# Kernel tuning notes

Hardware: AMD Instinct MI355X
Metric: run time of the kernel (lower is better)

The kernel has to match this reference:

```python
import jax, jax.numpy as jnp
import numpy as np

NUM_BITS = 8
SEQ, BATCH, INPUT, HIDDEN = 512, 256, 256, 256


def fake_quant(w):
    # symmetric per-tensor uniform fake-quantization with straight-through estimator
    qmax = 2.0 ** (NUM_BITS - 1) - 1.0
    scale = jnp.max(jnp.abs(w)) / qmax
    wq = jnp.round(w / scale) * scale
    return w + jax.lax.stop_gradient(wq - w)


def gru_cell(x, h, w_ih, w_hh, b_ih, b_hh):
    # x: [B, I], h: [B, H]; w_ih: [3H, I], w_hh: [3H, H]
    gi = x @ fake_quant(w_ih).T + b_ih  # [B, 3H]
    gh = h @ fake_quant(w_hh).T + b_hh  # [B, 3H]
    i_r, i_z, i_n = jnp.split(gi, 3, axis=-1)
    h_r, h_z, h_n = jnp.split(gh, 3, axis=-1)
    r = jax.nn.sigmoid(i_r + h_r)
    z = jax.nn.sigmoid(i_z + h_z)
    n = jnp.tanh(i_n + r * h_n)
    return (1.0 - z) * n + z * h


def setup_inputs() -> dict:
    key = jax.random.key(0)
    ks = jax.random.split(key, 9)
    s1 = 1.0 / np.sqrt(HIDDEN)
    inp = {
        "x": jax.random.normal(ks[0], (SEQ, BATCH, INPUT), dtype=jnp.float32),
        "h1": jnp.zeros((BATCH, HIDDEN), dtype=jnp.float32),
        "h2": jnp.zeros((BATCH, HIDDEN), dtype=jnp.float32),
        "w_ih1": jax.random.uniform(ks[1], (3 * HIDDEN, INPUT), jnp.float32, -s1, s1),
        "w_hh1": jax.random.uniform(ks[2], (3 * HIDDEN, HIDDEN), jnp.float32, -s1, s1),
        "b_ih1": jax.random.uniform(ks[3], (3 * HIDDEN,), jnp.float32, -s1, s1),
        "b_hh1": jax.random.uniform(ks[4], (3 * HIDDEN,), jnp.float32, -s1, s1),
        "w_ih2": jax.random.uniform(ks[5], (3 * HIDDEN, HIDDEN), jnp.float32, -s1, s1),
        "w_hh2": jax.random.uniform(ks[6], (3 * HIDDEN, HIDDEN), jnp.float32, -s1, s1),
        "b_ih2": jax.random.uniform(ks[7], (3 * HIDDEN,), jnp.float32, -s1, s1),
        "b_hh2": jax.random.uniform(ks[8], (3 * HIDDEN,), jnp.float32, -s1, s1),
    }
    return inp


def reference(x, h1, h2, w_ih1, w_hh1, b_ih1, b_hh1, w_ih2, w_hh2, b_ih2, b_hh2):
    def step(carry, x_t):
        h1, h2 = carry
        h1 = gru_cell(x_t, h1, w_ih1, w_hh1, b_ih1, b_hh1)
        h2 = gru_cell(h1, h2, w_ih2, w_hh2, b_ih2, b_hh2)
        return (h1, h2), None

    (h1, h2), _ = jax.lax.scan(step, (h1, h2), x)
    return h2
```

## Files before the change

### kernel.cpp

```cpp
#include <hip/hip_runtime.h>
#include <hip/hip_fp16.h>
#include <cstdint>

typedef _Float16 half8 __attribute__((ext_vector_type(8)));
typedef _Float16 half4 __attribute__((ext_vector_type(4)));
typedef float f32x4 __attribute__((ext_vector_type(4)));

#define MFMA_F16 __builtin_amdgcn_mfma_f32_16x16x32_f16
#define PIN(x)   asm volatile("" : "+v"(x))
#define LD_RLX(p)   __hip_atomic_load((p),  __ATOMIC_RELAXED, __HIP_MEMORY_SCOPE_AGENT)
#define LD_ACQ(p)   __hip_atomic_load((p),  __ATOMIC_ACQUIRE, __HIP_MEMORY_SCOPE_AGENT)
#define ST_REL(p,v) __hip_atomic_store((p),(v), __ATOMIC_RELEASE, __HIP_MEMORY_SCOPE_AGENT)

__device__ __forceinline__ float fast_rcp(float x){
#if __has_builtin(__builtin_amdgcn_rcpf)
  return __builtin_amdgcn_rcpf(x);
#else
  return 1.0f/x;
#endif
}
__device__ __forceinline__ float fast_exp2(float x){
#if __has_builtin(__builtin_amdgcn_exp2f)
  return __builtin_amdgcn_exp2f(x);
#else
  return exp2f(x);
#endif
}
__device__ __forceinline__ float sigm_f(float x){
  return fast_rcp(1.0f + fast_exp2(-1.44269504f*x));
}
__device__ __forceinline__ float tanh_fast(float x){
  float e = fast_exp2(-2.88539008f*x);
  return fmaf(2.0f, fast_rcp(1.0f + e), -1.0f);
}

__device__ __forceinline__ void bar_weak(){
  asm volatile("s_waitcnt lgkmcnt(0)" ::: "memory");
  __builtin_amdgcn_s_barrier();
  asm volatile("" ::: "memory");
}
__device__ __forceinline__ void bar_strong(){
  asm volatile("s_waitcnt vmcnt(0) lgkmcnt(0)" ::: "memory");
  __builtin_amdgcn_s_barrier();
  asm volatile("" ::: "memory");
}

__device__ __forceinline__ half8 qfrag(const float* __restrict__ W, int tile,
                                       int kb, int l, float scale){
  int row = tile*16 + (l & 15);
  int k0  = kb*32 + (l >> 4)*8;
  const float4* p = (const float4*)&W[row*256 + k0];
  float4 a = p[0], b = p[1];
  half8 h;
  h[0] = (_Float16)(rintf(a.x/scale)*scale);
  h[1] = (_Float16)(rintf(a.y/scale)*scale);
  h[2] = (_Float16)(rintf(a.z/scale)*scale);
  h[3] = (_Float16)(rintf(a.w/scale)*scale);
  h[4] = (_Float16)(rintf(b.x/scale)*scale);
  h[5] = (_Float16)(rintf(b.y/scale)*scale);
  h[6] = (_Float16)(rintf(b.z/scale)*scale);
  h[7] = (_Float16)(rintf(b.w/scale)*scale);
  return h;
}

__global__ __launch_bounds__(256) void k_maxabs(
    const float* __restrict__ w0, const float* __restrict__ w1,
    const float* __restrict__ w2, const float* __restrict__ w3,
    int n, int* __restrict__ slots)
{
  const float* srcs[4] = {w0, w1, w2, w3};
  int m    = blockIdx.x >> 5;
  int part = blockIdx.x & 31;
  const float* w = srcs[m];
  float loc = 0.0f;
  for (int i = part*256 + threadIdx.x; i < n; i += 32*256)
    loc = fmaxf(loc, fabsf(w[i]));
  for (int off = 32; off; off >>= 1)
    loc = fmaxf(loc, __shfl_down(loc, off, 64));
  __shared__ float red[4];
  int wv = threadIdx.x >> 6;
  if ((threadIdx.x & 63) == 0) red[wv] = loc;
  __syncthreads();
  if (threadIdx.x == 0) {
    float mx = fmaxf(fmaxf(red[0], red[1]), fmaxf(red[2], red[3]));
    atomicMax(&slots[m], __float_as_int(mx));
  }
}

__global__ __launch_bounds__(256) void k_xcast(
    const float* __restrict__ x, _Float16* __restrict__ xh)
{
  int n = blockIdx.x*256 + threadIdx.x;
  int t   = n >> 13;
  int rem = n & 8191;
  int bg  = rem >> 5;
  int k8  = rem & 31;
  const float4* src = (const float4*)&x[((size_t)t*256 + bg)*256 + k8*8];
  float4 v0 = src[0], v1 = src[1];
  half8 hv;
  hv[0] = (_Float16)v0.x; hv[1] = (_Float16)v0.y;
  hv[2] = (_Float16)v0.z; hv[3] = (_Float16)v0.w;
  hv[4] = (_Float16)v1.x; hv[5] = (_Float16)v1.y;
  hv[6] = (_Float16)v1.z; hv[7] = (_Float16)v1.w;
  int bb = bg >> 4, b = bg & 15, kb = k8 >> 2, lane = (k8 & 3)*16 + b;
  *(half8*)&xh[(size_t)t*65536 + (size_t)bb*4096 + kb*512 + lane*8] = hv;
}

__global__ __launch_bounds__(512, 2) void k_pipe(
    const _Float16* __restrict__ xh,
    const float* __restrict__ wih1, const float* __restrict__ bih1,
    _Float16* __restrict__ gi1, const float* __restrict__ whh1,
    const float* __restrict__ bhh1, float* __restrict__ hc1,
    _Float16* __restrict__ h1seq,
    const float* __restrict__ wih2, const float* __restrict__ bih2,
    const float* __restrict__ bhh2, const float* __restrict__ whh2,
    float* __restrict__ hc2, _Float16* __restrict__ gi2,
    const int* __restrict__ slots,
    int* __restrict__ flag0, int* __restrict__ flag1,
    int* __restrict__ flag2, int* __restrict__ flag3)
{
  __shared__ __align__(16) _Float16 hl[2][4096];
  __shared__ __align__(16) _Float16 wn_l[16384];
  const int role = blockIdx.x;
  const int tid  = threadIdx.x;
  const int w = tid >> 6, l = tid & 63, q = l >> 4, c16 = l & 15;

  if (role >= 32) {
    const bool G1 = (role >= 64);
    const int id = G1 ? role - 64 : role - 32;
    const int bb = id >> 1, par = id & 1;
    const float*    Wsrc = G1 ? wih1  : wih2;
    const float*    bihp = G1 ? bih1  : bih2;
    const float*    bhhp = G1 ? bhh1  : bhh2;
    const _Float16* Asrc = G1 ? xh    : h1seq;
    _Float16*       gout = G1 ? gi1   : gi2;
    const float sc = __int_as_float(slots[G1 ? 0 : 2]) * (1.0f/127.0f);

    float bR[2], bZ[2], bN[2];
    half8 wr[2][8], wz[2][8], wn[2][8];
    #pragma unroll
    for (int nt = 0; nt < 2; nt++) {
      const int j = w*32 + nt*16 + c16;
      bR[nt] = bihp[j]       + bhhp[j];
      bZ[nt] = bihp[256 + j] + bhhp[256 + j];
      bN[nt] = bihp[512 + j];
      #pragma unroll
      for (int kb = 0; kb < 8; kb++) {
        wr[nt][kb] = qfrag(Wsrc,      2*w + nt, kb, l, sc);  PIN(wr[nt][kb]);
        wz[nt][kb] = qfrag(Wsrc, 16 + 2*w + nt, kb, l, sc);  PIN(wz[nt][kb]);
        wn[nt][kb] = qfrag(Wsrc, 32 + 2*w + nt, kb, l, sc);  PIN(wn[nt][kb]);
      }
    }

    for (int g = par; g < 32; g += 2) {
      const int t0 = g*16;
      if (tid == 0) {
        if (!G1) {
          while (LD_RLX(&flag1[bb]) < t0 + 16) __builtin_amdgcn_s_sleep(10);
          if (g >= 4)
            while (LD_RLX(&flag3[bb]) < (g - 3)*16) __builtin_amdgcn_s_sleep(10);
          (void)LD_ACQ(&flag1[bb]);
        } else if (g >= 4) {
          while (LD_RLX(&flag1[bb]) < (g - 3)*16) __builtin_amdgcn_s_sleep(10);
          (void)LD_ACQ(&flag1[bb]);
        }
      }
      __syncthreads();
      for (int t = t0; t < t0 + 16; t++) {
        const _Float16* ap = Asrc + (size_t)t*65536 + (size_t)bb*4096 + l*8;
        f32x4 aR[2], aZ[2], aN[2];
        #pragma unroll
        for (int nt = 0; nt < 2; nt++) {
          aR[nt] = (f32x4){0.f,0.f,0.f,0.f};
          aZ[nt] = (f32x4){0.f,0.f,0.f,0.f};
          aN[nt] = (f32x4){0.f,0.f,0.f,0.f};
        }
        #pragma unroll
        for (int kb = 0; kb < 8; kb++) {
          half8 a = *(const half8*)&ap[kb*512];
          #pragma unroll
          for (int nt = 0; nt < 2; nt++) {
            aR[nt] = MFMA_F16(a, wr[nt][kb], aR[nt], 0, 0, 0);
            aZ[nt] = MFMA_F16(a, wz[nt][kb], aZ[nt], 0, 0, 0);
            aN[nt] = MFMA_F16(a, wn[nt][kb], aN[nt], 0, 0, 0);
          }
        }
        const size_t trow = (size_t)(t & 63);
        #pragma unroll
        for (int nt = 0; nt < 2; nt++) {
          _Float16* op = gout + (trow*256 + (2*w + nt)*16 + bb)*768 + l*12;
          half4 vR, vZ, vN;
          #pragma unroll
          for (int i = 0; i < 4; i++) {
            vR[i] = (_Float16)(aR[nt][i] + bR[nt]);
            vZ[i] = (_Float16)(aZ[nt][i] + bZ[nt]);
            vN[i] = (_Float16)(aN[nt][i] + bN[nt]);
          }
          *(half4*)(op)     = vR;
          *(half4*)(op + 4) = vZ;
          *(half4*)(op + 8) = vN;
        }
      }
      __syncthreads();
      if (tid == 0) {
        if (G1) ST_REL(&flag0[bb*2 + par], t0 + 16);
        else    ST_REL(&flag2[bb*2 + par], t0 + 16);
      }
    }
    return;
  }

  const bool L1 = (role < 16);
  const int bb = L1 ? role : role - 16;
  const int b0 = bb * 16;
  const _Float16* gi = L1 ? gi1 : gi2;
  const float* Wf    = L1 ? whh1 : whh2;
  const float* bhh   = L1 ? bhh1 : bhh2;
  float* hcarry      = L1 ? hc1 : hc2;
  const float sc     = __int_as_float(slots[L1 ? 1 : 3]) * (1.0f/127.0f);

  {
    int n = tid*8;
    int b = n >> 8, k = n & 255;
    const float4* s4 = (const float4*)&hcarry[(size_t)(b0 + b)*256 + k];
    float4 v0 = s4[0], v1 = s4[1];
    half8 hv;
    hv[0] = (_Float16)v0.x; hv[1] = (_Float16)v0.y;
    hv[2] = (_Float16)v0.z; hv[3] = (_Float16)v0.w;
    hv[4] = (_Float16)v1.x; hv[5] = (_Float16)v1.y;
    hv[6] = (_Float16)v1.z; hv[7] = (_Float16)v1.w;
    *(half8*)&hl[0][(k >> 5)*512 + (((k >> 3) & 3)*16 + b)*8] = hv;
  }

  float bN[2];
  float hprev[2][4];
  half8 wr[2][8], wz[2][8], wn[2][6];
  int   wr_off[2];
  int   gil[2];
  #pragma unroll
  for (int nt = 0; nt < 2; nt++) {
    const int j = w*32 + nt*16 + c16;
    bN[nt] = bhh[512 + j];
    #pragma unroll
    for (int i = 0; i < 4; i++)
      hprev[nt][i] = hcarry[(size_t)(b0 + q*4 + i)*256 + j];
    #pragma unroll
    for (int kb = 0; kb < 8; kb++) {
      wr[nt][kb] = qfrag(Wf,      2*w + nt, kb, l, sc);  PIN(wr[nt][kb]);
      wz[nt][kb] = qfrag(Wf, 16 + 2*w + nt, kb, l, sc);  PIN(wz[nt][kb]);
    }
    #pragma unroll
    for (int kb = 2; kb < 8; kb++) {
      wn[nt][kb-2] = qfrag(Wf, 32 + 2*w + nt, kb, l, sc);  PIN(wn[nt][kb-2]);
    }
    #pragma unroll
    for (int kb = 0; kb < 2; kb++)
      *(half8*)&wn_l[((w*2 + nt)*2 + kb)*512 + l*8] =
          qfrag(Wf, 32 + 2*w + nt, kb, l, sc);
    wr_off[nt] = (j >> 5)*512 + ((j >> 3) & 3)*128 + (j & 7);
    gil[nt]    = ((2*w + nt)*16 + bb)*768 + l*12;
  }
  _Float16* hq = L1 ? (h1seq + (size_t)bb*4096 + tid*8) : (_Float16*)nullptr;

  __syncthreads();
  half4 pR[2], pZ[2], pN[2];
  int cur = 0;
  for (int t = 0; t < 512; t++) {
    if ((t & 15) == 0) {
      if (tid == 0) {
        int* f = L1 ? &flag0[bb*2 + ((t >> 4) & 1)]
                    : &flag2[bb*2 + ((t >> 4) & 1)];
        while (LD_RLX(f) < t + 16) __builtin_amdgcn_s_sleep(10);
        (void)LD_ACQ(f);
      }
      __syncthreads();
      const int tm = t & 63;
      const _Float16* gbase = gi + (size_t)tm*196608;
      #pragma unroll
      for (int nt = 0; nt < 2; nt++) {
        const _Float16* gp = gbase + gil[nt];
        pR[nt] = *(const half4*)(gp);
        pZ[nt] = *(const half4*)(gp + 4);
        pN[nt] = *(const half4*)(gp + 8);
      }
    }
    half4 vR[2], vZ[2], vN[2];
    #pragma unroll
    for (int nt = 0; nt < 2; nt++) {
      vR[nt] = pR[nt]; vZ[nt] = pZ[nt]; vN[nt] = pN[nt];
    }

    f32x4 aR[2], aZ[2], aN[2];
    #pragma unroll
    for (int nt = 0; nt < 2; nt++) {
      aR[nt] = (f32x4){0.f,0.f,0.f,0.f};
      aZ[nt] = (f32x4){0.f,0.f,0.f,0.f};
      aN[nt] = (f32x4){0.f,0.f,0.f,0.f};
    }
    #pragma unroll
    for (int kb = 0; kb < 8; kb++) {
      half8 a = *(const half8*)&hl[cur][kb*512 + l*8];
      #pragma unroll
      for (int nt = 0; nt < 2; nt++) {
        half8 bn = (kb < 2)
            ? *(const half8*)&wn_l[((w*2 + nt)*2 + kb)*512 + l*8]
            : wn[nt][kb-2];
        aR[nt] = MFMA_F16(a, wr[nt][kb], aR[nt], 0, 0, 0);
        aZ[nt] = MFMA_F16(a, wz[nt][kb], aZ[nt], 0, 0, 0);
        aN[nt] = MFMA_F16(a, bn,         aN[nt], 0, 0, 0);
      }
    }

    if (((t + 1) & 15) != 0) {
      const int tn = (t + 1) & 63;
      const _Float16* gbase = gi + (size_t)tn*196608;
      #pragma unroll
      for (int nt = 0; nt < 2; nt++) {
        const _Float16* gp = gbase + gil[nt];
        pR[nt] = *(const half4*)(gp);
        pZ[nt] = *(const half4*)(gp + 4);
        pN[nt] = *(const half4*)(gp + 8);
      }
    }

    const int nxt = cur ^ 1;
    #pragma unroll
    for (int nt = 0; nt < 2; nt++) {
      #pragma unroll
      for (int i = 0; i < 4; i++) {
        float r  = sigm_f(aR[nt][i] + (float)vR[nt][i]);
        float z  = sigm_f(aZ[nt][i] + (float)vZ[nt][i]);
        float nn = tanh_fast((float)vN[nt][i] + r*(aN[nt][i] + bN[nt]));
        float hp = nn + z*(hprev[nt][i] - nn);
        hprev[nt][i] = hp;
        hl[nxt][wr_off[nt] + (q*4 + i)*8] = (_Float16)hp;
      }
    }

    if ((t & 15) == 0 && t > 0) {
      bar_strong();
      if (tid == 0) {
        if (L1) ST_REL(&flag1[bb], t);
        else    ST_REL(&flag3[bb], t);
      }
    } else {
      bar_weak();
    }
    if (L1)
      *(half8*)&hq[(size_t)t*65536] = *(const half8*)&hl[nxt][tid*8];
    cur = nxt;
  }
  bar_strong();
  if (tid == 0) {
    if (L1) ST_REL(&flag1[bb], 512);
    else    ST_REL(&flag3[bb], 512);
  }

  #pragma unroll
  for (int nt = 0; nt < 2; nt++) {
    const int j = w*32 + nt*16 + c16;
    #pragma unroll
    for (int i = 0; i < 4; i++)
      hcarry[(size_t)(b0 + q*4 + i)*256 + j] = hprev[nt][i];
  }
}

extern "C" void kernel_launch(void* const* d_in, const int* in_sizes, int n_in,
                              void* d_out, int out_size, void* d_ws, size_t ws_size,
                              hipStream_t stream)
{
  const float* x     = (const float*)d_in[0];
  const float* h1_0  = (const float*)d_in[1];
  const float* h2_0  = (const float*)d_in[2];
  const float* w_ih1 = (const float*)d_in[3];
  const float* w_hh1 = (const float*)d_in[4];
  const float* b_ih1 = (const float*)d_in[5];
  const float* b_hh1 = (const float*)d_in[6];
  const float* w_ih2 = (const float*)d_in[7];
  const float* w_hh2 = (const float*)d_in[8];
  const float* b_ih2 = (const float*)d_in[9];
  const float* b_hh2 = (const float*)d_in[10];

  char* ws = (char*)d_ws;
  size_t off = 0;
  auto alloc = [&](size_t bytes) -> void* {
    void* p = ws + off; off += (bytes + 255) & ~(size_t)255; return p;
  };
  int*      slots   = (int*)     alloc(16);
  float*    hc1     = (float*)   alloc(256*256*4);
  float*    hc2     = (float*)   alloc(256*256*4);
  int*      flag0   = (int*)     alloc(32*4);
  int*      flag1   = (int*)     alloc(16*4);
  int*      flag2   = (int*)     alloc(32*4);
  int*      flag3   = (int*)     alloc(16*4);
  _Float16* gi1     = (_Float16*)alloc((size_t)64*393216);
  _Float16* h1seq   = (_Float16*)alloc((size_t)512*131072);
  _Float16* gi2     = (_Float16*)alloc((size_t)64*393216);
  _Float16* xhbuf   = (_Float16*)alloc((size_t)512*131072);

  k_maxabs<<<128, 256, 0, stream>>>(w_ih1, w_hh1, w_ih2, w_hh2, 196608, slots);
  k_xcast <<<16384, 256, 0, stream>>>(x, xhbuf);
  (void)hipMemcpyAsync(hc1, h1_0, 256*256*4, hipMemcpyDeviceToDevice, stream);
  (void)hipMemcpyAsync(hc2, h2_0, 256*256*4, hipMemcpyDeviceToDevice, stream);

  k_pipe<<<96, 512, 0, stream>>>(xhbuf, w_ih1, b_ih1, gi1, w_hh1, b_hh1,
                                 hc1, h1seq, w_ih2, b_ih2, b_hh2, w_hh2,
                                 hc2, gi2, slots, flag0, flag1, flag2, flag3);

  (void)hipMemcpyAsync(d_out, hc2, 256*256*4, hipMemcpyDeviceToDevice, stream);
}
```

Measured before the change: 1.338 ms.

## Process two batch groups per recurrent block with interleaved MFMA and gate phases

Each recurrent block now handles two 16-row batch groups instead of one, halving the recurrent block count (grid goes from 96 to 80). The MFMA phase of one group is interleaved with the gate/activation phase of the other so that matrix and transcendental work can overlap across the serial time loop. All of W_n now lives in registers, so the LDS copy of part of it is dropped. In exchange each block does twice the per-step work on fewer CUs, uses more registers, and waits on two producer flags.

```diff
diff --git a/kernel.cpp b/kernel.cpp
--- a/kernel.cpp
+++ b/kernel.cpp
@@ -119,15 +119,14 @@
     int* __restrict__ flag0, int* __restrict__ flag1,
     int* __restrict__ flag2, int* __restrict__ flag3)
 {
-  __shared__ __align__(16) _Float16 hl[2][4096];
-  __shared__ __align__(16) _Float16 wn_l[16384];
+  __shared__ __align__(16) _Float16 hl[8192];
   const int role = blockIdx.x;
   const int tid  = threadIdx.x;
   const int w = tid >> 6, l = tid & 63, q = l >> 4, c16 = l & 15;
 
-  if (role >= 32) {
-    const bool G1 = (role >= 64);
-    const int id = G1 ? role - 64 : role - 32;
+  if (role >= 16) {
+    const bool G1 = (role >= 48);
+    const int id = G1 ? role - 48 : role - 16;
     const int bb = id >> 1, par = id & 1;
     const float*    Wsrc = G1 ? wih1  : wih2;
     const float*    bihp = G1 ? bih1  : bih2;
@@ -210,87 +209,66 @@
     return;
   }
 
-  const bool L1 = (role < 16);
-  const int bb = L1 ? role : role - 16;
-  const int b0 = bb * 16;
+  const bool L1 = (role < 8);
+  const int pb = L1 ? role*2 : (role - 8)*2;
   const _Float16* gi = L1 ? gi1 : gi2;
   const float* Wf    = L1 ? whh1 : whh2;
   const float* bhh   = L1 ? bhh1 : bhh2;
   float* hcarry      = L1 ? hc1 : hc2;
   const float sc     = __int_as_float(slots[L1 ? 1 : 3]) * (1.0f/127.0f);
+  int* fAcq = L1 ? flag0 : flag2;
+  int* fPub = L1 ? flag1 : flag3;
+  _Float16* hl0 = hl;
+  _Float16* hl1 = hl + 4096;
 
   {
     int n = tid*8;
     int b = n >> 8, k = n & 255;
-    const float4* s4 = (const float4*)&hcarry[(size_t)(b0 + b)*256 + k];
-    float4 v0 = s4[0], v1 = s4[1];
-    half8 hv;
-    hv[0] = (_Float16)v0.x; hv[1] = (_Float16)v0.y;
-    hv[2] = (_Float16)v0.z; hv[3] = (_Float16)v0.w;
-    hv[4] = (_Float16)v1.x; hv[5] = (_Float16)v1.y;
-    hv[6] = (_Float16)v1.z; hv[7] = (_Float16)v1.w;
-    *(half8*)&hl[0][(k >> 5)*512 + (((k >> 3) & 3)*16 + b)*8] = hv;
+    int dst = (k >> 5)*512 + (((k >> 3) & 3)*16 + b)*8;
+    #pragma unroll
+    for (int bbi = 0; bbi < 2; bbi++) {
+      const float4* s4 = (const float4*)&hcarry[(size_t)((pb+bbi)*16 + b)*256 + k];
+      float4 v0 = s4[0], v1 = s4[1];
+      half8 hv;
+      hv[0] = (_Float16)v0.x; hv[1] = (_Float16)v0.y;
+      hv[2] = (_Float16)v0.z; hv[3] = (_Float16)v0.w;
+      hv[4] = (_Float16)v1.x; hv[5] = (_Float16)v1.y;
+      hv[6] = (_Float16)v1.z; hv[7] = (_Float16)v1.w;
+      *(half8*)&hl[bbi*4096 + dst] = hv;
+    }
   }
 
   float bN[2];
-  float hprev[2][4];
-  half8 wr[2][8], wz[2][8], wn[2][6];
+  float hprev[2][2][4];
+  half8 wr[2][8], wz[2][8], wn[2][8];
   int   wr_off[2];
-  int   gil[2];
+  int   gil[2][2];
   #pragma unroll
   for (int nt = 0; nt < 2; nt++) {
     const int j = w*32 + nt*16 + c16;
     bN[nt] = bhh[512 + j];
     #pragma unroll
-    for (int i = 0; i < 4; i++)
-      hprev[nt][i] = hcarry[(size_t)(b0 + q*4 + i)*256 + j];
+    for (int bbi = 0; bbi < 2; bbi++) {
+      #pragma unroll
+      for (int i = 0; i < 4; i++)
+        hprev[bbi][nt][i] = hcarry[(size_t)((pb+bbi)*16 + q*4 + i)*256 + j];
+      gil[bbi][nt] = ((2*w + nt)*16 + (pb+bbi))*768 + l*12;
+    }
     #pragma unroll
     for (int kb = 0; kb < 8; kb++) {
       wr[nt][kb] = qfrag(Wf,      2*w + nt, kb, l, sc);  PIN(wr[nt][kb]);
       wz[nt][kb] = qfrag(Wf, 16 + 2*w + nt, kb, l, sc);  PIN(wz[nt][kb]);
-    }
-    #pragma unroll
-    for (int kb = 2; kb < 8; kb++) {
-      wn[nt][kb-2] = qfrag(Wf, 32 + 2*w + nt, kb, l, sc);  PIN(wn[nt][kb-2]);
-    }
-    #pragma unroll
-    for (int kb = 0; kb < 2; kb++)
-      *(half8*)&wn_l[((w*2 + nt)*2 + kb)*512 + l*8] =
-          qfrag(Wf, 32 + 2*w + nt, kb, l, sc);
+      wn[nt][kb] = qfrag(Wf, 32 + 2*w + nt, kb, l, sc);  PIN(wn[nt][kb]);
+    }
     wr_off[nt] = (j >> 5)*512 + ((j >> 3) & 3)*128 + (j & 7);
-    gil[nt]    = ((2*w + nt)*16 + bb)*768 + l*12;
-  }
-  _Float16* hq = L1 ? (h1seq + (size_t)bb*4096 + tid*8) : (_Float16*)nullptr;
-
-  __syncthreads();
-  half4 pR[2], pZ[2], pN[2];
-  int cur = 0;
-  for (int t = 0; t < 512; t++) {
-    if ((t & 15) == 0) {
-      if (tid == 0) {
-        int* f = L1 ? &flag0[bb*2 + ((t >> 4) & 1)]
-                    : &flag2[bb*2 + ((t >> 4) & 1)];
-        while (LD_RLX(f) < t + 16) __builtin_amdgcn_s_sleep(10);
-        (void)LD_ACQ(f);
-      }
-      __syncthreads();
-      const int tm = t & 63;
-      const _Float16* gbase = gi + (size_t)tm*196608;
-      #pragma unroll
-      for (int nt = 0; nt < 2; nt++) {
-        const _Float16* gp = gbase + gil[nt];
-        pR[nt] = *(const half4*)(gp);
-        pZ[nt] = *(const half4*)(gp + 4);
-        pN[nt] = *(const half4*)(gp + 8);
-      }
-    }
-    half4 vR[2], vZ[2], vN[2];
-    #pragma unroll
-    for (int nt = 0; nt < 2; nt++) {
-      vR[nt] = pR[nt]; vZ[nt] = pZ[nt]; vN[nt] = pN[nt];
-    }
-
-    f32x4 aR[2], aZ[2], aN[2];
+  }
+  _Float16* hq0 = L1 ? (h1seq + (size_t)pb*4096     + tid*8) : (_Float16*)nullptr;
+  _Float16* hq1 = L1 ? (h1seq + (size_t)(pb+1)*4096 + tid*8) : (_Float16*)nullptr;
+
+  f32x4 aR0[2], aZ0[2], aN0[2], aR1[2], aZ1[2], aN1[2];
+  half4 pR0[2], pZ0[2], pN0[2], pR1[2], pZ1[2], pN1[2];
+
+  auto mfma_ph = [&](const _Float16* hlx, f32x4* aR, f32x4* aZ, f32x4* aN){
     #pragma unroll
     for (int nt = 0; nt < 2; nt++) {
       aR[nt] = (f32x4){0.f,0.f,0.f,0.f};
@@ -299,69 +277,96 @@
     }
     #pragma unroll
     for (int kb = 0; kb < 8; kb++) {
-      half8 a = *(const half8*)&hl[cur][kb*512 + l*8];
+      half8 a = *(const half8*)&hlx[kb*512 + l*8];
       #pragma unroll
       for (int nt = 0; nt < 2; nt++) {
-        half8 bn = (kb < 2)
-            ? *(const half8*)&wn_l[((w*2 + nt)*2 + kb)*512 + l*8]
-            : wn[nt][kb-2];
         aR[nt] = MFMA_F16(a, wr[nt][kb], aR[nt], 0, 0, 0);
         aZ[nt] = MFMA_F16(a, wz[nt][kb], aZ[nt], 0, 0, 0);
-        aN[nt] = MFMA_F16(a, bn,         aN[nt], 0, 0, 0);
-      }
-    }
-
-    if (((t + 1) & 15) != 0) {
-      const int tn = (t + 1) & 63;
-      const _Float16* gbase = gi + (size_t)tn*196608;
-      #pragma unroll
-      for (int nt = 0; nt < 2; nt++) {
-        const _Float16* gp = gbase + gil[nt];
-        pR[nt] = *(const half4*)(gp);
-        pZ[nt] = *(const half4*)(gp + 4);
-        pN[nt] = *(const half4*)(gp + 8);
-      }
-    }
-
-    const int nxt = cur ^ 1;
+        aN[nt] = MFMA_F16(a, wn[nt][kb], aN[nt], 0, 0, 0);
+      }
+    }
+  };
+  auto gate_ph = [&](int bbi, _Float16* hlx, f32x4* aR, f32x4* aZ, f32x4* aN,
+                     half4* pR, half4* pZ, half4* pN){
     #pragma unroll
     for (int nt = 0; nt < 2; nt++) {
       #pragma unroll
       for (int i = 0; i < 4; i++) {
-        float r  = sigm_f(aR[nt][i] + (float)vR[nt][i]);
-        float z  = sigm_f(aZ[nt][i] + (float)vZ[nt][i]);
-        float nn = tanh_fast((float)vN[nt][i] + r*(aN[nt][i] + bN[nt]));
-        float hp = nn + z*(hprev[nt][i] - nn);
-        hprev[nt][i] = hp;
-        hl[nxt][wr_off[nt] + (q*4 + i)*8] = (_Float16)hp;
-      }
-    }
-
+        float r  = sigm_f(aR[nt][i] + (float)pR[nt][i]);
+        float z  = sigm_f(aZ[nt][i] + (float)pZ[nt][i]);
+        float nn = tanh_fast((float)pN[nt][i] + r*(aN[nt][i] + bN[nt]));
+        float hp = nn + z*(hprev[bbi][nt][i] - nn);
+        hprev[bbi][nt][i] = hp;
+        hlx[wr_off[nt] + (q*4 + i)*8] = (_Float16)hp;
+      }
+    }
+  };
+  auto pref = [&](int bbi, int t, half4* pR, half4* pZ, half4* pN){
+    const _Float16* gbase = gi + (size_t)(t & 63)*196608;
+    #pragma unroll
+    for (int nt = 0; nt < 2; nt++) {
+      const _Float16* gp = gbase + gil[bbi][nt];
+      pR[nt] = *(const half4*)(gp);
+      pZ[nt] = *(const half4*)(gp + 4);
+      pN[nt] = *(const half4*)(gp + 8);
+    }
+  };
+
+  __syncthreads();
+  if (tid == 0) {
+    while (LD_RLX(&fAcq[pb*2])     < 16) __builtin_amdgcn_s_sleep(10);
+    while (LD_RLX(&fAcq[(pb+1)*2]) < 16) __builtin_amdgcn_s_sleep(10);
+    (void)LD_ACQ(&fAcq[pb*2]);
+  }
+  __syncthreads();
+  pref(0, 0, pR0, pZ0, pN0);
+  mfma_ph(hl0, aR0, aZ0, aN0);
+  bar_weak();
+
+  for (int t = 0; t < 512; t++) {
+    if ((t & 15) == 0 && t > 0) {
+      if (tid == 0) {
+        int par = (t >> 4) & 1;
+        while (LD_RLX(&fAcq[pb*2 + par])     < t + 16) __builtin_amdgcn_s_sleep(10);
+        while (LD_RLX(&fAcq[(pb+1)*2 + par]) < t + 16) __builtin_amdgcn_s_sleep(10);
+        (void)LD_ACQ(&fAcq[pb*2 + par]);
+      }
+      __syncthreads();
+      pref(0, t, pR0, pZ0, pN0);
+    }
+    if (L1 && t > 0)
+      *(half8*)&hq1[(size_t)(t-1)*65536] = *(const half8*)&hl1[tid*8];
+    gate_ph(0, hl0, aR0, aZ0, aN0, pR0, pZ0, pN0);
+    mfma_ph(hl1, aR1, aZ1, aN1);
+    pref(1, t, pR1, pZ1, pN1);
     if ((t & 15) == 0 && t > 0) {
       bar_strong();
-      if (tid == 0) {
-        if (L1) ST_REL(&flag1[bb], t);
-        else    ST_REL(&flag3[bb], t);
-      }
+      if (tid == 0) { ST_REL(&fPub[pb], t); ST_REL(&fPub[pb+1], t); }
     } else {
       bar_weak();
     }
+
     if (L1)
-      *(half8*)&hq[(size_t)t*65536] = *(const half8*)&hl[nxt][tid*8];
-    cur = nxt;
-  }
+      *(half8*)&hq0[(size_t)t*65536] = *(const half8*)&hl0[tid*8];
+    if (t < 511) mfma_ph(hl0, aR0, aZ0, aN0);
+    gate_ph(1, hl1, aR1, aZ1, aN1, pR1, pZ1, pN1);
+    if (t < 511 && ((t+1) & 15) != 0) pref(0, t+1, pR0, pZ0, pN0);
+    bar_weak();
+  }
+  if (L1)
+    *(half8*)&hq1[(size_t)511*65536] = *(const half8*)&hl1[tid*8];
   bar_strong();
-  if (tid == 0) {
-    if (L1) ST_REL(&flag1[bb], 512);
-    else    ST_REL(&flag3[bb], 512);
-  }
+  if (tid == 0) { ST_REL(&fPub[pb], 512); ST_REL(&fPub[pb+1], 512); }
 
   #pragma unroll
-  for (int nt = 0; nt < 2; nt++) {
-    const int j = w*32 + nt*16 + c16;
-    #pragma unroll
-    for (int i = 0; i < 4; i++)
-      hcarry[(size_t)(b0 + q*4 + i)*256 + j] = hprev[nt][i];
+  for (int bbi = 0; bbi < 2; bbi++) {
+    #pragma unroll
+    for (int nt = 0; nt < 2; nt++) {
+      const int j = w*32 + nt*16 + c16;
+      #pragma unroll
+      for (int i = 0; i < 4; i++)
+        hcarry[(size_t)((pb+bbi)*16 + q*4 + i)*256 + j] = hprev[bbi][nt][i];
+    }
   }
 }
 
@@ -403,7 +408,7 @@
   (void)hipMemcpyAsync(hc1, h1_0, 256*256*4, hipMemcpyDeviceToDevice, stream);
   (void)hipMemcpyAsync(hc2, h2_0, 256*256*4, hipMemcpyDeviceToDevice, stream);
 
-  k_pipe<<<96, 512, 0, stream>>>(xhbuf, w_ih1, b_ih1, gi1, w_hh1, b_hh1,
+  k_pipe<<<80, 512, 0, stream>>>(xhbuf, w_ih1, b_ih1, gi1, w_hh1, b_hh1,
                                  hc1, h1seq, w_ih2, b_ih2, b_hh2, w_hh2,
                                  hc2, gi2, slots, flag0, flag1, flag2, flag3);
 
```

Result: slower. 5.255 ms (+292.6%).
